# Kernel optimization log

Measured on AMD Instinct MI355X. Metric: run time of the kernel, lower is better.

The kernel has to match this reference:

```python
import jax, jax.numpy as jnp
import numpy as np

B, S, H, E, TOPK = 4, 2048, 2048, 8, 2


def setup_inputs() -> dict:
    key = jax.random.key(0)
    ks = jax.random.split(key, 3)
    scale_g = 1.0 / np.sqrt(H)
    scale_e = 1.0 / np.sqrt(H)
    return {
        "x": jax.random.normal(ks[0], (B, S, H), dtype=jnp.float32),
        "Wg": jax.random.normal(ks[1], (H, E), dtype=jnp.float32) * scale_g,
        "bg": jnp.zeros((E,), dtype=jnp.float32),
        "We": jax.random.normal(ks[2], (E, H, H), dtype=jnp.float32) * scale_e,
        "be": jnp.zeros((E, H), dtype=jnp.float32),
        "top_k": TOPK,
    }


def reference(x, Wg, bg, We, be, top_k):
    # x: [B, S, H]
    b, s, h = x.shape
    e = Wg.shape[1]
    tok = x.reshape(-1, h)                      # [T, H]
    logits = tok @ Wg + bg                      # [T, E]
    scores = jax.nn.softmax(logits, axis=-1)    # [T, E]
    _, idx = jax.lax.top_k(scores, top_k)       # [T, top_k]
    # per-expert membership mask: token routed to expert iff expert in its top-k
    mask = (idx[:, :, None] == jnp.arange(e)[None, None, :]).any(axis=1)  # [T, E]
    out = jnp.zeros_like(tok)
    for eid in range(e):  # small fixed expert loop (structurally distinct weights)
        gate = jnp.where(mask[:, eid], scores[:, eid], 0.0)  # [T]
        # dense per-expert layer; tokens not routed contribute exactly zero,
        # matching the torch gather -> dense -> scatter-add combine
        out = out + gate[:, None] * (tok @ We[eid] + be[eid])
    return out.reshape(b, s, h)
```

## Files before the change

### kernel.cpp

```cpp
#include <hip/hip_runtime.h>
#include <hip/hip_bf16.h>

#define TOK 8192
#define HD 2048
#define NE 8
#define KTOP 2
#define NSLOT (TOK * KTOP)
#define NCHUNK (TOK / 256)

typedef __attribute__((ext_vector_type(8))) short bf16x8;
typedef __attribute__((ext_vector_type(4))) float f32x4;

#define GLDS16(g, l) __builtin_amdgcn_global_load_lds( \
    (const __attribute__((address_space(1))) void*)(g), \
    (__attribute__((address_space(3))) void*)(l), 16, 0, 0)

__device__ __forceinline__ unsigned short f2bf(float f) {
  union { float f; unsigned u; } v; v.f = f;
  unsigned r = v.u + 0x7fffu + ((v.u >> 16) & 1u);
  return (unsigned short)(r >> 16);
}
__device__ __forceinline__ float bf2f(unsigned short b) {
  union { unsigned u; float f; } v; v.u = ((unsigned)b) << 16;
  return v.f;
}

__global__ __launch_bounds__(256) void route_wconv_kernel(
    const float* __restrict__ x, const float* __restrict__ Wg, const float* __restrict__ bg,
    const float* __restrict__ We,
    int* __restrict__ eidx2, float* __restrict__ gate2,
    unsigned short* __restrict__ xbf, unsigned short* __restrict__ Wt) {
  __shared__ union {
    struct { float xs[HD]; float red[4][NE]; } r;
    float tile[64][65];
  } sm;
  int bid = blockIdx.x;
  int tid = threadIdx.x;

  if (bid & 1) {
    int i = bid >> 1;
    int e = i >> 10;
    int rem = i & 1023;
    int k0 = (rem >> 5) * 64, n0 = (rem & 31) * 64;
    const float* src = We + ((size_t)e * HD + k0) * HD + n0;
#pragma unroll
    for (int it = 0; it < 4; it++) {
      int f = tid + it * 256;
      int r = f >> 4, c4 = (f & 15) * 4;
      float4 v = *(const float4*)(src + (size_t)r * HD + c4);
      sm.tile[r][c4 + 0] = v.x; sm.tile[r][c4 + 1] = v.y;
      sm.tile[r][c4 + 2] = v.z; sm.tile[r][c4 + 3] = v.w;
    }
    __syncthreads();
    unsigned short* dst = Wt + ((size_t)e * HD + n0) * HD + k0;
#pragma unroll
    for (int it = 0; it < 2; it++) {
      int s = tid + it * 256;
      int n = s >> 3, k8 = (s & 7) * 8;
      union { bf16x8 v; unsigned short us[8]; } o;
#pragma unroll
      for (int j = 0; j < 8; j++) o.us[j] = f2bf(sm.tile[k8 + j][n]);
      *(bf16x8*)(dst + (size_t)n * HD + k8) = o.v;
    }
    return;
  }

  int t = bid >> 1;
  const float4* xr = (const float4*)(x + (size_t)t * HD);
  float4 a = xr[tid * 2], b = xr[tid * 2 + 1];
  union { bf16x8 v; unsigned short s[8]; } o;
  o.s[0] = f2bf(a.x); o.s[1] = f2bf(a.y); o.s[2] = f2bf(a.z); o.s[3] = f2bf(a.w);
  o.s[4] = f2bf(b.x); o.s[5] = f2bf(b.y); o.s[6] = f2bf(b.z); o.s[7] = f2bf(b.w);
  *(bf16x8*)(xbf + (size_t)t * HD + tid * 8) = o.v;
  *(float4*)(sm.r.xs + tid * 8) = a;
  *(float4*)(sm.r.xs + tid * 8 + 4) = b;
  __syncthreads();

  float acc[NE];
#pragma unroll
  for (int e = 0; e < NE; e++) acc[e] = 0.f;
#pragma unroll
  for (int i = 0; i < HD / 256; i++) {
    int k = tid + i * 256;
    float v = sm.r.xs[k];
    const float4* wr = (const float4*)(Wg + (size_t)k * NE);
    float4 w0 = wr[0], w1 = wr[1];
    acc[0] += v * w0.x; acc[1] += v * w0.y; acc[2] += v * w0.z; acc[3] += v * w0.w;
    acc[4] += v * w1.x; acc[5] += v * w1.y; acc[6] += v * w1.z; acc[7] += v * w1.w;
  }
#pragma unroll
  for (int e = 0; e < NE; e++) {
    float v = acc[e];
#pragma unroll
    for (int s = 32; s > 0; s >>= 1) v += __shfl_xor(v, s, 64);
    acc[e] = v;
  }
  int lane = tid & 63, w = tid >> 6;
  if (lane == 0)
#pragma unroll
    for (int e = 0; e < NE; e++) sm.r.red[w][e] = acc[e];
  __syncthreads();
  if (tid == 0) {
    float lg[NE];
#pragma unroll
    for (int e = 0; e < NE; e++)
      lg[e] = sm.r.red[0][e] + sm.r.red[1][e] + sm.r.red[2][e] + sm.r.red[3][e] + bg[e];
    float m = lg[0];
#pragma unroll
    for (int e = 1; e < NE; e++) m = fmaxf(m, lg[e]);
    float p[NE], d = 0.f;
#pragma unroll
    for (int e = 0; e < NE; e++) { p[e] = __expf(lg[e] - m); d += p[e]; }
    float inv = 1.f / d;
    int b0 = 0;
#pragma unroll
    for (int e = 1; e < NE; e++) if (lg[e] > lg[b0]) b0 = e;
    int b1 = (b0 == 0) ? 1 : 0;
#pragma unroll
    for (int e = 0; e < NE; e++) if (e != b0 && lg[e] > lg[b1]) b1 = e;
    eidx2[t * 2 + 0] = b0; gate2[t * 2 + 0] = p[b0] * inv;
    eidx2[t * 2 + 1] = b1; gate2[t * 2 + 1] = p[b1] * inv;
  }
}

__global__ __launch_bounds__(256) void hist_kernel(const int* __restrict__ eidx2,
                                                   int* __restrict__ hist) {
  __shared__ int h[4][NE];
  int b = blockIdx.x, tid = threadIdx.x;
  int lane = tid & 63, w = tid >> 6;
  int t = b * 256 + tid;
  int e0 = eidx2[t * 2], e1 = eidx2[t * 2 + 1];
#pragma unroll
  for (int ee = 0; ee < NE; ee++) {
    unsigned long long m0 = __ballot(e0 == ee);
    unsigned long long m1 = __ballot(e1 == ee);
    if (lane == 0) h[w][ee] = __popcll(m0) + __popcll(m1);
  }
  __syncthreads();
  if (tid < NE) hist[b * NE + tid] = h[0][tid] + h[1][tid] + h[2][tid] + h[3][tid];
}

__global__ __launch_bounds__(256) void assign_kernel(
    const int* __restrict__ eidx2, const float* __restrict__ gate2,
    const int* __restrict__ hist, int* __restrict__ cnt,
    int* __restrict__ slot_tok, float* __restrict__ slot_gate, int* __restrict__ tok_slot) {
  __shared__ int wcnt[2][4][NE];
  __shared__ int tot[NE], cbs[NE], cb[NE];
  int b = blockIdx.x;
  int tid = threadIdx.x;
  int lane = tid & 63, w = tid >> 6;
  if (tid < NE) {
    int s = 0, base = 0;
    for (int bb = 0; bb < NCHUNK; bb++) {
      if (bb == b) base = s;
      s += hist[bb * NE + tid];
    }
    tot[tid] = s; cbs[tid] = base;
    if (b == 0) cnt[tid] = s;
  }
  int t = b * 256 + tid;
  int e0 = eidx2[t * 2], e1 = eidx2[t * 2 + 1];
  unsigned long long lt = (1ull << lane) - 1ull;
  int r0 = 0, r1 = 0;
#pragma unroll
  for (int ee = 0; ee < NE; ee++) {
    unsigned long long m0 = __ballot(e0 == ee);
    unsigned long long m1 = __ballot(e1 == ee);
    if (e0 == ee) r0 = __popcll(m0 & lt);
    if (e1 == ee) r1 = __popcll(m1 & lt);
    if (lane == 0) { wcnt[0][w][ee] = __popcll(m0); wcnt[1][w][ee] = __popcll(m1); }
  }
  __syncthreads();
  if (tid == 0) {
    int o = 0;
#pragma unroll
    for (int e = 0; e < NE; e++) { cb[e] = cbs[e] + o; o += tot[e]; }
  }
  __syncthreads();
  int base0 = 0, base1 = 0;
#pragma unroll
  for (int p = 0; p < 8; p++) {
    int c0 = wcnt[p >> 2][p & 3][e0];
    int c1 = wcnt[p >> 2][p & 3][e1];
    if (p < w) base0 += c0;
    if (p < 4 + w) base1 += c1;
  }
  int s0 = cb[e0] + base0 + r0;
  int s1 = cb[e1] + base1 + r1;
  slot_tok[s0] = t; slot_gate[s0] = gate2[t * 2 + 0];
  slot_tok[s1] = t; slot_gate[s1] = gate2[t * 2 + 1];
  tok_slot[t * 2 + 0] = s0;
  tok_slot[t * 2 + 1] = s1;
}

#define BM 128
#define BN 128
#define BK 32
#define EPS 72

__global__ __launch_bounds__(256) void moe_gemm(
    const unsigned short* __restrict__ xbf, const unsigned short* __restrict__ Wt,
    const int* __restrict__ cnt, const int* __restrict__ slot_tok,
    const float* __restrict__ be, unsigned short* __restrict__ Ybf) {
  int bid = blockIdx.x;
  int e = bid >> 10;
  int rem = bid & 1023;
  int mt = rem >> 4, nt = rem & 15;
  int off = 0, c = 0;
#pragma unroll
  for (int i = 0; i < NE; i++) { int ci = cnt[i]; if (i < e) off += ci; if (i == e) c = ci; }
  if (mt * BM >= c) return;
  int row0 = off + mt * BM;
  int n0 = nt * BN;

  __shared__ unsigned short Sm[2][BM * BK + BN * BK];

  int tid = threadIdx.x;
  int lane = tid & 63, w = tid >> 6;
  int wm = w & 1, wn = w >> 1;
  int quad = lane >> 4, l16 = lane & 15;

  int srow = lane >> 2;
  int sq   = lane & 3;
  int ra0 = w * 32 + srow, ra1 = ra0 + 16;
  int sl0 = min(row0 + ra0, NSLOT - 1);
  int sl1 = min(row0 + ra1, NSLOT - 1);
  size_t ta0 = (size_t)slot_tok[sl0], ta1 = (size_t)slot_tok[sl1];
  const unsigned short* gA0 = xbf + ta0 * HD + sq * 8;
  const unsigned short* gA1 = xbf + ta1 * HD + sq * 8;
  const unsigned short* gB0 = Wt + ((size_t)e * HD + n0 + ra0) * HD + sq * 8;
  const unsigned short* gB1 = Wt + ((size_t)e * HD + n0 + ra1) * HD + sq * 8;
  int oA0 = (w * 32) * BK;
  int oA1 = (w * 32 + 16) * BK;
  int oB0 = BM * BK + (w * 32) * BK;
  int oB1 = BM * BK + (w * 32 + 16) * BK;

  int pa_off = (wm * 64 + l16) * BK + quad * 8;
  int pb_off = BM * BK + (wn * 64 + l16) * BK + quad * 8;

  f32x4 acc[4][4] = {};

  GLDS16(gA0, &Sm[0][oA0]);
  GLDS16(gA1, &Sm[0][oA1]);
  GLDS16(gB0, &Sm[0][oB0]);
  GLDS16(gB1, &Sm[0][oB1]);
  gA0 += BK; gA1 += BK; gB0 += BK; gB1 += BK;
  __syncthreads();

  int cur = 0;
  for (int kt = 0; kt < HD / BK; ++kt) {
    if (kt + 1 < HD / BK) {
      unsigned short* nb = Sm[cur ^ 1];
      GLDS16(gA0, nb + oA0);
      GLDS16(gA1, nb + oA1);
      GLDS16(gB0, nb + oB0);
      GLDS16(gB1, nb + oB1);
      gA0 += BK; gA1 += BK; gB0 += BK; gB1 += BK;
    }
    const unsigned short* base = Sm[cur];
    bf16x8 af[4], bfr[4];
#pragma unroll
    for (int i = 0; i < 4; i++) {
      af[i]  = *(const bf16x8*)(base + pa_off + i * 16 * BK);
      bfr[i] = *(const bf16x8*)(base + pb_off + i * 16 * BK);
    }
#pragma unroll
    for (int im = 0; im < 4; im++)
#pragma unroll
      for (int in = 0; in < 4; in++)
        acc[im][in] = __builtin_amdgcn_mfma_f32_16x16x32_bf16(af[im], bfr[in], acc[im][in], 0, 0, 0);
    __syncthreads();
    cur ^= 1;
  }

  float bias[4];
#pragma unroll
  for (int in = 0; in < 4; in++)
    bias[in] = be[e * HD + n0 + wn * 64 + in * 16 + l16];

  unsigned short* reg = &Sm[0][0] + w * (16 * EPS);
  int rrow = lane >> 2;
  int rcol = (lane & 3) * 16;
#pragma unroll
  for (int im = 0; im < 4; im++) {
#pragma unroll
    for (int in = 0; in < 4; in++)
#pragma unroll
      for (int r = 0; r < 4; r++)
        reg[(quad * 4 + r) * EPS + in * 16 + l16] = f2bf(acc[im][in][r] + bias[in]);
    __syncthreads();
    int gr = mt * BM + wm * 64 + im * 16 + rrow;
    if (gr < c) {
      bf16x8 v0 = *(const bf16x8*)(reg + rrow * EPS + rcol);
      bf16x8 v1 = *(const bf16x8*)(reg + rrow * EPS + rcol + 8);
      unsigned short* dst = Ybf + (size_t)(off + gr) * HD + n0 + wn * 64 + rcol;
      *(bf16x8*)dst = v0;
      *(bf16x8*)(dst + 8) = v1;
    }
    __syncthreads();
  }
}

__global__ __launch_bounds__(256) void combine_kernel(
    const unsigned short* __restrict__ Ybf, const int* __restrict__ tok_slot,
    const float* __restrict__ slot_gate, float* __restrict__ out) {
  int c8 = threadIdx.x * 8;
#pragma unroll
  for (int i = 0; i < 4; i++) {
    int t = blockIdx.x * 4 + i;
    int s0 = tok_slot[t * 2], s1 = tok_slot[t * 2 + 1];
    float g0 = slot_gate[s0], g1 = slot_gate[s1];
    union { bf16x8 v; unsigned short s[8]; } y0, y1;
    y0.v = *(const bf16x8*)(Ybf + (size_t)s0 * HD + c8);
    y1.v = *(const bf16x8*)(Ybf + (size_t)s1 * HD + c8);
    float4 o0, o1;
    o0.x = g0 * bf2f(y0.s[0]) + g1 * bf2f(y1.s[0]);
    o0.y = g0 * bf2f(y0.s[1]) + g1 * bf2f(y1.s[1]);
    o0.z = g0 * bf2f(y0.s[2]) + g1 * bf2f(y1.s[2]);
    o0.w = g0 * bf2f(y0.s[3]) + g1 * bf2f(y1.s[3]);
    o1.x = g0 * bf2f(y0.s[4]) + g1 * bf2f(y1.s[4]);
    o1.y = g0 * bf2f(y0.s[5]) + g1 * bf2f(y1.s[5]);
    o1.z = g0 * bf2f(y0.s[6]) + g1 * bf2f(y1.s[6]);
    o1.w = g0 * bf2f(y0.s[7]) + g1 * bf2f(y1.s[7]);
    float4* dst = (float4*)(out + (size_t)t * HD + c8);
    dst[0] = o0;
    dst[1] = o1;
  }
}

extern "C" void kernel_launch(void* const* d_in, const int* in_sizes, int n_in,
                              void* d_out, int out_size, void* d_ws, size_t ws_size,
                              hipStream_t stream) {
  const float* x  = (const float*)d_in[0];
  const float* Wg = (const float*)d_in[1];
  const float* bg = (const float*)d_in[2];
  const float* We = (const float*)d_in[3];
  const float* be = (const float*)d_in[4];
  float* out = (float*)d_out;

  char* ws = (char*)d_ws;
  int* cnt        = (int*)ws;
  int* hist       = (int*)(ws + 256);
  int* eidx2       = (int*)(ws + 4096);
  float* gate2     = (float*)(ws + 4096 + NSLOT * 4);
  int* slot_tok    = (int*)(ws + 4096 + 2 * NSLOT * 4);
  float* slot_gate = (float*)(ws + 4096 + 3 * NSLOT * 4);
  int* tok_slot    = (int*)(ws + 4096 + 4 * NSLOT * 4);
  unsigned short* xbf = (unsigned short*)(ws + 8192 + 5 * NSLOT * 4);
  unsigned short* Wt  = xbf + (size_t)TOK * HD;
  unsigned short* Ybf = Wt + (size_t)NE * HD * HD;

  route_wconv_kernel<<<2 * TOK, 256, 0, stream>>>(x, Wg, bg, We, eidx2, gate2, xbf, Wt);
  hist_kernel<<<NCHUNK, 256, 0, stream>>>(eidx2, hist);
  assign_kernel<<<NCHUNK, 256, 0, stream>>>(eidx2, gate2, hist, cnt, slot_tok, slot_gate, tok_slot);
  moe_gemm<<<NE * 64 * 16, 256, 0, stream>>>(xbf, Wt, cnt, slot_tok, be, Ybf);
  combine_kernel<<<TOK / 4, 256, 0, stream>>>(Ybf, tok_slot, slot_gate, out);
}
```

Measured before the change: 489.3 us.

## Enlarge MoE GEMM tiles to 256x256x64 with swizzled LDS and interleaved prefetch

Replaces the 128x128x32 expert GEMM with a 512-thread 256x256x64 tile kernel. It XOR-swizzles the LDS layout to avoid bank conflicts and splits the next-tile global-to-LDS loads into chunks interleaved with MFMA phases. It also uses setprio around the MFMAs and remaps block IDs so blocks sharing expert weights run close together. The goals are more data reuse per LDS byte, better overlap of loads with compute, and better L2 locality. The cost is 128KB of LDS per block, which limits occupancy to one block per CU, plus tighter manual vmcnt synchronization.

```diff
diff --git a/kernel.cpp b/kernel.cpp
--- a/kernel.cpp
+++ b/kernel.cpp
@@ -193,103 +193,128 @@
   tok_slot[t * 2 + 1] = s1;
 }
 
-#define BM 128
-#define BN 128
-#define BK 32
+#define BMG 256
+#define BNG 256
+#define BKG 64
+#define NTG (HD / BKG)
 #define EPS 72
 
-__global__ __launch_bounds__(256) void moe_gemm(
+#define STAGEA(b, j) GLDS16(gA[j], &Sm[b][aDst + (j) * 512])
+#define STAGEB(b, j) GLDS16(gB + (size_t)((j) * 8) * HD, &Sm[b][bDst + (j) * 512])
+
+#define PHASE(p, STAGES) do { \
+    bf16x8 a00 = *(const bf16x8*)(SA + rdA + (2*(p)+0) * 1024 + s0); \
+    bf16x8 a01 = *(const bf16x8*)(SA + rdA + (2*(p)+0) * 1024 + s1); \
+    bf16x8 a10 = *(const bf16x8*)(SA + rdA + (2*(p)+1) * 1024 + s0); \
+    bf16x8 a11 = *(const bf16x8*)(SA + rdA + (2*(p)+1) * 1024 + s1); \
+    STAGES; \
+    __builtin_amdgcn_s_setprio(1); \
+    _Pragma("unroll") \
+    for (int in = 0; in < 4; in++) { \
+      acc[2*(p)][in]   = __builtin_amdgcn_mfma_f32_16x16x32_bf16(a00, b0[in], acc[2*(p)][in], 0, 0, 0); \
+      acc[2*(p)][in]   = __builtin_amdgcn_mfma_f32_16x16x32_bf16(a01, b1[in], acc[2*(p)][in], 0, 0, 0); \
+      acc[2*(p)+1][in] = __builtin_amdgcn_mfma_f32_16x16x32_bf16(a10, b0[in], acc[2*(p)+1][in], 0, 0, 0); \
+      acc[2*(p)+1][in] = __builtin_amdgcn_mfma_f32_16x16x32_bf16(a11, b1[in], acc[2*(p)+1][in], 0, 0, 0); \
+    } \
+    __builtin_amdgcn_s_setprio(0); \
+  } while (0)
+
+__global__ __launch_bounds__(512, 2) void moe_gemm256(
     const unsigned short* __restrict__ xbf, const unsigned short* __restrict__ Wt,
     const int* __restrict__ cnt, const int* __restrict__ slot_tok,
     const float* __restrict__ be, unsigned short* __restrict__ Ybf) {
-  int bid = blockIdx.x;
-  int e = bid >> 10;
-  int rem = bid & 1023;
-  int mt = rem >> 4, nt = rem & 15;
+  int d = blockIdx.x;
+  int o = (d & 7) * 512 + (d >> 3);
+  int e = o >> 9;
+  int nt = (o >> 6) & 7;
+  int mt = o & 63;
   int off = 0, c = 0;
 #pragma unroll
   for (int i = 0; i < NE; i++) { int ci = cnt[i]; if (i < e) off += ci; if (i == e) c = ci; }
-  if (mt * BM >= c) return;
-  int row0 = off + mt * BM;
-  int n0 = nt * BN;
-
-  __shared__ unsigned short Sm[2][BM * BK + BN * BK];
+  if (mt * BMG >= c) return;
+  int row0 = off + mt * BMG;
+  int n0 = nt * BNG;
+
+  __shared__ unsigned short Sm[2][2 * 16384];
 
   int tid = threadIdx.x;
   int lane = tid & 63, w = tid >> 6;
   int wm = w & 1, wn = w >> 1;
   int quad = lane >> 4, l16 = lane & 15;
 
-  int srow = lane >> 2;
-  int sq   = lane & 3;
-  int ra0 = w * 32 + srow, ra1 = ra0 + 16;
-  int sl0 = min(row0 + ra0, NSLOT - 1);
-  int sl1 = min(row0 + ra1, NSLOT - 1);
-  size_t ta0 = (size_t)slot_tok[sl0], ta1 = (size_t)slot_tok[sl1];
-  const unsigned short* gA0 = xbf + ta0 * HD + sq * 8;
-  const unsigned short* gA1 = xbf + ta1 * HD + sq * 8;
-  const unsigned short* gB0 = Wt + ((size_t)e * HD + n0 + ra0) * HD + sq * 8;
-  const unsigned short* gB1 = Wt + ((size_t)e * HD + n0 + ra1) * HD + sq * 8;
-  int oA0 = (w * 32) * BK;
-  int oA1 = (w * 32 + 16) * BK;
-  int oB0 = BM * BK + (w * 32) * BK;
-  int oB1 = BM * BK + (w * 32 + 16) * BK;
-
-  int pa_off = (wm * 64 + l16) * BK + quad * 8;
-  int pb_off = BM * BK + (wn * 64 + l16) * BK + quad * 8;
-
-  f32x4 acc[4][4] = {};
-
-  GLDS16(gA0, &Sm[0][oA0]);
-  GLDS16(gA1, &Sm[0][oA1]);
-  GLDS16(gB0, &Sm[0][oB0]);
-  GLDS16(gB1, &Sm[0][oB1]);
-  gA0 += BK; gA1 += BK; gB0 += BK; gB1 += BK;
-  __syncthreads();
-
-  int cur = 0;
-  for (int kt = 0; kt < HD / BK; ++kt) {
-    if (kt + 1 < HD / BK) {
-      unsigned short* nb = Sm[cur ^ 1];
-      GLDS16(gA0, nb + oA0);
-      GLDS16(gA1, nb + oA1);
-      GLDS16(gB0, nb + oB0);
-      GLDS16(gB1, nb + oB1);
-      gA0 += BK; gA1 += BK; gB0 += BK; gB1 += BK;
-    }
-    const unsigned short* base = Sm[cur];
-    bf16x8 af[4], bfr[4];
-#pragma unroll
-    for (int i = 0; i < 4; i++) {
-      af[i]  = *(const bf16x8*)(base + pa_off + i * 16 * BK);
-      bfr[i] = *(const bf16x8*)(base + pb_off + i * 16 * BK);
-    }
-#pragma unroll
-    for (int im = 0; im < 4; im++)
-#pragma unroll
-      for (int in = 0; in < 4; in++)
-        acc[im][in] = __builtin_amdgcn_mfma_f32_16x16x32_bf16(af[im], bfr[in], acc[im][in], 0, 0, 0);
-    __syncthreads();
-    cur ^= 1;
-  }
-
-  float bias[4];
+  int lrow = lane >> 3;
+  int kswz = ((lane & 7) ^ lrow) * 8;
+  const unsigned short* gA[4];
+#pragma unroll
+  for (int j = 0; j < 4; j++) {
+    int sl = min(row0 + w * 32 + j * 8 + lrow, NSLOT - 1);
+    gA[j] = xbf + (size_t)slot_tok[sl] * HD + kswz;
+  }
+  const unsigned short* gB = Wt + ((size_t)e * HD + n0 + w * 32 + lrow) * HD + kswz;
+  int aDst = (w * 32) * 64;
+  int bDst = 16384 + (w * 32) * 64;
+
+  int rdA = (wm * 128 + l16) * 64;
+  int rdB = 16384 + (wn * 64 + l16) * 64;
+  int s0 = ((quad) ^ (l16 & 7)) * 8;
+  int s1 = ((4 + quad) ^ (l16 & 7)) * 8;
+
+  f32x4 acc[8][4] = {};
+
+#pragma unroll
+  for (int j = 0; j < 4; j++) STAGEA(0, j);
+#pragma unroll
+  for (int j = 0; j < 4; j++) STAGEB(0, j);
+#pragma unroll
+  for (int j = 0; j < 4; j++) gA[j] += BKG;
+  gB += BKG;
+
+  for (int kt = 0; kt < NTG; ++kt) {
+    const int buf = kt & 1, nb = buf ^ 1;
+    const unsigned short* SA = &Sm[buf][0];
+    const bool pf = (kt < NTG - 1);
+    __builtin_amdgcn_s_barrier();
+    __builtin_amdgcn_sched_barrier(0);
+    if (pf) { STAGEA(nb, 0); STAGEA(nb, 1); }
+    __builtin_amdgcn_sched_barrier(0);
+    if (pf) asm volatile("s_waitcnt vmcnt(2)" ::: "memory");
+    else    asm volatile("s_waitcnt vmcnt(0)" ::: "memory");
+    __builtin_amdgcn_sched_barrier(0);
+    __builtin_amdgcn_s_barrier();
+    __builtin_amdgcn_sched_barrier(0);
+
+    bf16x8 b0[4], b1[4];
+#pragma unroll
+    for (int in = 0; in < 4; in++) {
+      b0[in] = *(const bf16x8*)(SA + rdB + in * 1024 + s0);
+      b1[in] = *(const bf16x8*)(SA + rdB + in * 1024 + s1);
+    }
+    PHASE(0, (void)0);
+    PHASE(1, if (pf) { STAGEA(nb, 2); STAGEA(nb, 3); });
+    PHASE(2, if (pf) { STAGEB(nb, 0); STAGEB(nb, 1); });
+    PHASE(3, if (pf) { STAGEB(nb, 2); STAGEB(nb, 3); });
+#pragma unroll
+    for (int j = 0; j < 4; j++) gA[j] += BKG;
+    gB += BKG;
+  }
+
+  float biasr[4];
 #pragma unroll
   for (int in = 0; in < 4; in++)
-    bias[in] = be[e * HD + n0 + wn * 64 + in * 16 + l16];
+    biasr[in] = be[e * HD + n0 + wn * 64 + in * 16 + l16];
 
   unsigned short* reg = &Sm[0][0] + w * (16 * EPS);
   int rrow = lane >> 2;
   int rcol = (lane & 3) * 16;
 #pragma unroll
-  for (int im = 0; im < 4; im++) {
+  for (int im = 0; im < 8; im++) {
 #pragma unroll
     for (int in = 0; in < 4; in++)
 #pragma unroll
       for (int r = 0; r < 4; r++)
-        reg[(quad * 4 + r) * EPS + in * 16 + l16] = f2bf(acc[im][in][r] + bias[in]);
+        reg[(quad * 4 + r) * EPS + in * 16 + l16] = f2bf(acc[im][in][r] + biasr[in]);
     __syncthreads();
-    int gr = mt * BM + wm * 64 + im * 16 + rrow;
+    int gr = mt * BMG + wm * 128 + im * 16 + rrow;
     if (gr < c) {
       bf16x8 v0 = *(const bf16x8*)(reg + rrow * EPS + rcol);
       bf16x8 v1 = *(const bf16x8*)(reg + rrow * EPS + rcol + 8);
@@ -353,6 +378,6 @@
   route_wconv_kernel<<<2 * TOK, 256, 0, stream>>>(x, Wg, bg, We, eidx2, gate2, xbf, Wt);
   hist_kernel<<<NCHUNK, 256, 0, stream>>>(eidx2, hist);
   assign_kernel<<<NCHUNK, 256, 0, stream>>>(eidx2, gate2, hist, cnt, slot_tok, slot_gate, tok_slot);
-  moe_gemm<<<NE * 64 * 16, 256, 0, stream>>>(xbf, Wt, cnt, slot_tok, be, Ybf);
+  moe_gemm256<<<NE * 64 * 8, 512, 0, stream>>>(xbf, Wt, cnt, slot_tok, be, Ybf);
   combine_kernel<<<TOK / 4, 256, 0, stream>>>(Ybf, tok_slot, slot_gate, out);
 }
```

After: 461.1 us. -5.8%, faster.
